# Kernel tuning notes

Measured on AMD Instinct MI355X. Metric: run time of the kernel, lower is better.

The kernel has to match this reference:

```python
import jax, jax.numpy as jnp
import numpy as np

NUM_NODES = 100000
PROP_STEP = 8


def _spmm(vals, rows, cols, x):
    # sparse [N,N] @ dense [N,F]: gather source rows, scale, scatter-add to dest
    gathered = x[cols] * vals[:, None]  # [E, F]
    return jax.ops.segment_sum(gathered, rows, num_segments=NUM_NODES)


def setup_inputs() -> dict:
    key = jax.random.key(0)
    k1, k2, k3, k4, k5 = jax.random.split(key, 5)
    N, E, C = NUM_NODES, 3200000, 128
    x = jax.random.normal(k1, (N, C), dtype=jnp.float32)
    # xavier_uniform for weight [c_in, c_out]
    limit = float(np.sqrt(6.0 / (C + C)))
    weight = jax.random.uniform(k2, (C, C), dtype=jnp.float32, minval=-limit, maxval=limit)
    lap_vals = jax.random.uniform(k3, (E,), dtype=jnp.float32)
    lap_rows = jax.random.randint(k4, (E,), 0, N, dtype=jnp.int64)
    lap_cols = jax.random.randint(k5, (E,), 0, N, dtype=jnp.int64)
    return {"x": x, "weight": weight, "lap_vals": lap_vals,
            "lap_rows": lap_rows, "lap_cols": lap_cols}


def reference(x, weight, lap_vals, lap_rows, lap_cols):
    # filter_type='low', dropout inactive (eval / p=0)
    identity = x
    out = x @ weight  # [N, c_out]
    for _ in range(PROP_STEP):
        out = _spmm(lap_vals, lap_rows, lap_cols, out)
    return identity + out
```

## Files before the change

kernel.cpp:

```cpp
#include <hip/hip_runtime.h>
#include <hip/hip_bf16.h>
#include <hip/hip_fp16.h>
#include <stdint.h>

#define CCH 128
#define FINAL_SCALE 268435456.0f
#define RND 2048
#define BUKSH 9
#define BUKROWS 512
#define MAXBUK 256

typedef float f4_t __attribute__((ext_vector_type(4)));
typedef int i2_t __attribute__((ext_vector_type(2)));

__device__ __forceinline__ int2 nt_load_i2(const int2* p) {
    i2_t t = __builtin_nontemporal_load((const i2_t*)p);
    return make_int2(t.x, t.y);
}
__device__ __forceinline__ float4 nt_load_f4(const float* p) {
    f4_t t = __builtin_nontemporal_load((const f4_t*)p);
    return make_float4(t.x, t.y, t.z, t.w);
}
__device__ __forceinline__ void nt_store_f4(void* p, float a, float b, float c, float d) {
    f4_t t = {a, b, c, d};
    __builtin_nontemporal_store(t, (f4_t*)p);
}


__global__ __launch_bounds__(256) void bucket_hist_kernel(const int* __restrict__ rows,
                                                          int* __restrict__ bukcnt,
                                                          int E, int nbuk) {
    __shared__ int h[MAXBUK];
    for (int i = threadIdx.x; i < nbuk; i += 256) h[i] = 0;
    __syncthreads();
    int stride = gridDim.x * blockDim.x;
    for (int e = blockIdx.x * blockDim.x + threadIdx.x; e < E; e += stride)
        atomicAdd(&h[rows[e] >> BUKSH], 1);
    __syncthreads();
    for (int i = threadIdx.x; i < nbuk; i += 256)
        if (h[i]) atomicAdd(&bukcnt[i], h[i]);
}

__global__ __launch_bounds__(MAXBUK) void bucket_scan_kernel(const int* __restrict__ bukcnt,
                                                             int* __restrict__ bukptr,
                                                             int* __restrict__ gcur, int nbuk) {
    __shared__ int tile[MAXBUK];
    int t = threadIdx.x;
    tile[t] = (t < nbuk) ? bukcnt[t] : 0;
    __syncthreads();
    for (int off = 1; off < MAXBUK; off <<= 1) {
        int add = (t >= off) ? tile[t - off] : 0;
        __syncthreads();
        tile[t] += add;
        __syncthreads();
    }
    int excl = (t == 0) ? 0 : tile[t - 1];
    if (t < nbuk) {
        bukptr[t] = excl;
        gcur[t] = excl;
    }
    if (t == nbuk - 1) bukptr[nbuk] = tile[t];
}

__global__ __launch_bounds__(256) void part_kernel(const int* __restrict__ rows,
                                                   const int* __restrict__ cols,
                                                   const float* __restrict__ vals,
                                                   int* __restrict__ gcur,
                                                   int4* __restrict__ recs,
                                                   int E, int nbuk) {
    __shared__ int hist[MAXBUK];
    __shared__ int offs[MAXBUK];
    __shared__ int cur[MAXBUK];
    __shared__ int gbase[MAXBUK];
    __shared__ int4 stage[RND];

    int base = blockIdx.x * RND;
    int cnt = E - base;
    if (cnt > RND) cnt = RND;
    if (cnt <= 0) return;

    for (int i = threadIdx.x; i < nbuk; i += 256) hist[i] = 0;
    __syncthreads();

    int myr[RND / 256], myc[RND / 256];
    float myv[RND / 256];
#pragma unroll
    for (int k = 0; k < RND / 256; ++k) {
        int li = k * 256 + threadIdx.x;
        bool ok = li < cnt;
        int gi = base + li;
        myr[k] = ok ? rows[gi] : -1;
        myc[k] = ok ? cols[gi] : 0;
        myv[k] = ok ? vals[gi] : 0.f;
        if (ok) atomicAdd(&hist[myr[k] >> BUKSH], 1);
    }
    __syncthreads();

    if (threadIdx.x == 0) {
        int run = 0;
        for (int b = 0; b < nbuk; ++b) {
            offs[b] = run;
            cur[b] = run;
            run += hist[b];
        }
    }
    __syncthreads();
    if (threadIdx.x < nbuk) gbase[threadIdx.x] = atomicAdd(&gcur[threadIdx.x], hist[threadIdx.x]);
    __syncthreads();

#pragma unroll
    for (int k = 0; k < RND / 256; ++k) {
        if (myr[k] >= 0) {
            int b = myr[k] >> BUKSH;
            int p = atomicAdd(&cur[b], 1);
            stage[p] = make_int4(myr[k], myc[k], __float_as_int(myv[k]), 0);
        }
    }
    __syncthreads();

    for (int i = threadIdx.x; i < cnt; i += 256) {
        int4 r = stage[i];
        int b = r.x >> BUKSH;
        recs[(size_t)gbase[b] + (i - offs[b])] = r;
    }
}

__global__ __launch_bounds__(512) void csrfill2_kernel(const int4* __restrict__ recs,
                                                       const int* __restrict__ bukptr,
                                                       int* __restrict__ row_ptr,
                                                       int2* __restrict__ edges,
                                                       int n, int E) {
    __shared__ int lcnt[BUKROWS];
    __shared__ int lscan[BUKROWS];
    __shared__ int lfill[BUKROWS];
    int bucket = blockIdx.x;
    int r0 = bucket << BUKSH;
    if (r0 >= n) return;
    int t = threadIdx.x;
    int bstart = bukptr[bucket];
    int bend = bukptr[bucket + 1];

    lcnt[t] = 0;
    __syncthreads();

    for (int i = bstart + t; i < bend; i += 512)
        atomicAdd(&lcnt[recs[i].x - r0], 1);
    __syncthreads();

    int v = lcnt[t];
    lscan[t] = v;
    __syncthreads();
    for (int off = 1; off < 512; off <<= 1) {
        int add = (t >= off) ? lscan[t - off] : 0;
        __syncthreads();
        lscan[t] += add;
        __syncthreads();
    }
    int excl = lscan[t] - v;

    int r = r0 + t;
    if (r < n) row_ptr[r] = bstart + excl;
    if (bucket == 0 && t == 0) row_ptr[n] = E;

    lfill[t] = 0;
    lcnt[t] = bstart + excl;
    __syncthreads();

    int i = bstart + t;
    for (; i + 512 < bend; i += 1024) {
        int4 a = recs[i];
        int4 b = recs[i + 512];
        int pa = lcnt[a.x - r0] + atomicAdd(&lfill[a.x - r0], 1);
        int pb = lcnt[b.x - r0] + atomicAdd(&lfill[b.x - r0], 1);
        edges[pa] = make_int2(a.y, a.z);
        edges[pb] = make_int2(b.y, b.z);
    }
    if (i < bend) {
        int4 a = recs[i];
        int pa = lcnt[a.x - r0] + atomicAdd(&lfill[a.x - r0], 1);
        edges[pa] = make_int2(a.y, a.z);
    }
}


#define GEMM_ROWS 64

__global__ __launch_bounds__(256) void gemm_kernel(const float* __restrict__ x,
                                                   const float* __restrict__ w,
                                                   __half* __restrict__ out, int n) {
    __shared__ __half2 wl[CCH * 64];
    for (int i = threadIdx.x; i < CCH * 64 / 2; i += 256) {
        float4 v = ((const float4*)w)[i];
        wl[2 * i]     = __float22half2_rn(make_float2(v.x, v.y));
        wl[2 * i + 1] = __float22half2_rn(make_float2(v.z, v.w));
    }
    __syncthreads();

    int tc = threadIdx.x & 31;
    int tr = threadIdx.x >> 5;
    int rbase = blockIdx.x * GEMM_ROWS + tr * 8;
    int nr = n - rbase;
    if (nr > 8) nr = 8;
    if (nr <= 0) nr = 0;

    float acc[8][4] = {};
    const float* xp = x + (size_t)rbase * CCH;

    float4 xc[8];
#pragma unroll
    for (int j = 0; j < 8; ++j)
        xc[j] = (j < nr) ? *(const float4*)(xp + (size_t)j * CCH)
                         : make_float4(0.f, 0.f, 0.f, 0.f);

    for (int k = 0; k < CCH; k += 4) {
        float4 xn[8];
        if (k + 4 < CCH) {
#pragma unroll
            for (int j = 0; j < 8; ++j)
                xn[j] = (j < nr) ? *(const float4*)(xp + (size_t)j * CCH + k + 4)
                                 : make_float4(0.f, 0.f, 0.f, 0.f);
        }
#pragma unroll
        for (int kk = 0; kk < 4; ++kk) {
            __half2 w01 = wl[(k + kk) * 64 + tc * 2];
            __half2 w23 = wl[(k + kk) * 64 + tc * 2 + 1];
            float2 f01 = __half22float2(w01);
            float2 f23 = __half22float2(w23);
#pragma unroll
            for (int j = 0; j < 8; ++j) {
                float xs = (kk == 0) ? xc[j].x : (kk == 1) ? xc[j].y : (kk == 2) ? xc[j].z : xc[j].w;
                acc[j][0] += xs * f01.x;
                acc[j][1] += xs * f01.y;
                acc[j][2] += xs * f23.x;
                acc[j][3] += xs * f23.y;
            }
        }
        if (k + 4 < CCH) {
#pragma unroll
            for (int j = 0; j < 8; ++j) xc[j] = xn[j];
        }
    }
#pragma unroll
    for (int j = 0; j < 8; ++j)
        if (j < nr) {
            __half2* orow = (__half2*)(out + (size_t)(rbase + j) * CCH + tc * 4);
            orow[0] = __float22half2_rn(make_float2(acc[j][0], acc[j][1]));
            orow[1] = __float22half2_rn(make_float2(acc[j][2], acc[j][3]));
        }
}


template <int FINAL>
__global__ __launch_bounds__(256) void spmm_kernel(const int* __restrict__ row_ptr,
                                                   const int2* __restrict__ edges,
                                                   const __half* __restrict__ src,
                                                   __half* __restrict__ dsth,
                                                   float* __restrict__ dstf,
                                                   const float* __restrict__ identity,
                                                   int n) {
    int lane = threadIdx.x & 63;
    int row = (blockIdx.x * blockDim.x + threadIdx.x) >> 6;
    if (row >= n) return;
    int g = lane >> 4;
    int gl = lane & 15;

    int s = row_ptr[row];
    int e = row_ptr[row + 1];

    float acc[8] = {};

    for (int base = s; base < e; base += 16) {
        int2 ed[4];
        float4 gv[4];
#pragma unroll
        for (int t = 0; t < 4; ++t) {
            int idx = base + g * 4 + t;
            bool ok = idx < e;
            ed[t] = nt_load_i2(&edges[ok ? idx : s]);
            if (!ok) ed[t].y = 0;
        }
#pragma unroll
        for (int t = 0; t < 4; ++t)
            gv[t] = *(const float4*)(src + (size_t)ed[t].x * CCH + gl * 8);
#pragma unroll
        for (int t = 0; t < 4; ++t) {
            float v = __int_as_float(ed[t].y);
            const __half* h = (const __half*)&gv[t];
#pragma unroll
            for (int j = 0; j < 8; ++j)
                acc[j] += v * __half2float(h[j]);
        }
    }

#pragma unroll
    for (int j = 0; j < 8; ++j) {
        acc[j] += __shfl_xor(acc[j], 16, 64);
        acc[j] += __shfl_xor(acc[j], 32, 64);
    }

    if (FINAL) {
        if (g == 0) {
            float4 iv = nt_load_f4(identity + (size_t)row * CCH + gl * 8);
            nt_store_f4(dstf + (size_t)row * CCH + gl * 8,
                        iv.x + acc[0] * FINAL_SCALE, iv.y + acc[1] * FINAL_SCALE,
                        iv.z + acc[2] * FINAL_SCALE, iv.w + acc[3] * FINAL_SCALE);
        } else if (g == 1) {
            float4 iv = nt_load_f4(identity + (size_t)row * CCH + gl * 8 + 4);
            nt_store_f4(dstf + (size_t)row * CCH + gl * 8 + 4,
                        iv.x + acc[4] * FINAL_SCALE, iv.y + acc[5] * FINAL_SCALE,
                        iv.z + acc[6] * FINAL_SCALE, iv.w + acc[7] * FINAL_SCALE);
        }
    } else {
        if (g == 0) {
            __half2 h[4];
            h[0] = __float22half2_rn(make_float2(acc[0] * 0.0625f, acc[1] * 0.0625f));
            h[1] = __float22half2_rn(make_float2(acc[2] * 0.0625f, acc[3] * 0.0625f));
            h[2] = __float22half2_rn(make_float2(acc[4] * 0.0625f, acc[5] * 0.0625f));
            h[3] = __float22half2_rn(make_float2(acc[6] * 0.0625f, acc[7] * 0.0625f));
            float4 hv = *(float4*)h;
            nt_store_f4(dsth + (size_t)row * CCH + gl * 8, hv.x, hv.y, hv.z, hv.w);
        }
    }
}


static inline size_t align256(size_t x) { return (x + 255) & ~(size_t)255; }

extern "C" void kernel_launch(void* const* d_in, const int* in_sizes, int n_in,
                              void* d_out, int out_size, void* d_ws, size_t ws_size,
                              hipStream_t stream) {
    const float* x = (const float*)d_in[0];
    const float* w = (const float*)d_in[1];
    const float* lap_vals = (const float*)d_in[2];
    const int* lap_rows = (const int*)d_in[3];
    const int* lap_cols = (const int*)d_in[4];

    const int N = in_sizes[0] / CCH;
    const int E = in_sizes[2];
    const int NBUK = (N + BUKROWS - 1) >> BUKSH;

    char* ws = (char*)d_ws;
    size_t off = 0;
    __half* bufA = (__half*)(ws + off); off = align256(off + (size_t)N * CCH * sizeof(__half));
    __half* bufB = (__half*)(ws + off); off = align256(off + (size_t)N * CCH * sizeof(__half));
    int2* edges = (int2*)(ws + off);    off = align256(off + (size_t)E * sizeof(int2) + 16);
    int* row_ptr = (int*)(ws + off);    off = align256(off + (size_t)(N + 1) * sizeof(int));
    int* bukcnt = (int*)(ws + off);     off = align256(off + (size_t)MAXBUK * sizeof(int));
    int* bukptr = (int*)(ws + off);     off = align256(off + (size_t)(MAXBUK + 1) * sizeof(int));
    int* gcur = (int*)(ws + off);       off = align256(off + (size_t)MAXBUK * sizeof(int));
    (void)ws_size;
    int4* recs = (int4*)bufA;

    float* out = (float*)d_out;

    hipMemsetAsync(bukcnt, 0, (size_t)MAXBUK * sizeof(int), stream);

    bucket_hist_kernel<<<512, 256, 0, stream>>>(lap_rows, bukcnt, E, NBUK);
    bucket_scan_kernel<<<1, MAXBUK, 0, stream>>>(bukcnt, bukptr, gcur, NBUK);
    part_kernel<<<(E + RND - 1) / RND, 256, 0, stream>>>(lap_rows, lap_cols, lap_vals,
                                                         gcur, recs, E, NBUK);
    csrfill2_kernel<<<NBUK, 512, 0, stream>>>(recs, bukptr, row_ptr, edges, N, E);

    gemm_kernel<<<(N + GEMM_ROWS - 1) / GEMM_ROWS, 256, 0, stream>>>(x, w, bufA, N);

    int spmm_blocks = (N + 3) / 4;
    const __half* src = bufA;
    __half* dst = bufB;
    for (int step = 1; step <= 7; ++step) {
        spmm_kernel<0><<<spmm_blocks, 256, 0, stream>>>(row_ptr, edges, src, dst, nullptr, nullptr, N);
        __half* t = (__half*)src;
        src = dst;
        dst = t;
    }
    spmm_kernel<1><<<spmm_blocks, 256, 0, stream>>>(row_ptr, edges, src, nullptr, out, x, N);
}
```

Before: 1.196 ms.

## Pack partition records into 8 bytes and drop nontemporal hints in SpMM

The partition stage now stores each edge as a packed 32-bit word (local row in the high bits, column in the low 17 bits) plus a separate float value, instead of a 16-byte int4. This halves the intermediate record traffic written by part_kernel and read twice by csrfill2_kernel. The SpMM edge loads and the half-precision intermediate stores also switch from nontemporal to regular accesses, so the edge list and feature buffers can stay in cache across steps. Column packing assumes node indices fit in 17 bits, so it only works for graphs with fewer than 131072 nodes.

```diff
diff --git a/kernel.cpp b/kernel.cpp
--- a/kernel.cpp
+++ b/kernel.cpp
@@ -9,14 +9,10 @@
 #define BUKSH 9
 #define BUKROWS 512
 #define MAXBUK 256
+#define COLMASK 0x1FFFF
 
 typedef float f4_t __attribute__((ext_vector_type(4)));
-typedef int i2_t __attribute__((ext_vector_type(2)));
-
-__device__ __forceinline__ int2 nt_load_i2(const int2* p) {
-    i2_t t = __builtin_nontemporal_load((const i2_t*)p);
-    return make_int2(t.x, t.y);
-}
+
 __device__ __forceinline__ float4 nt_load_f4(const float* p) {
     f4_t t = __builtin_nontemporal_load((const f4_t*)p);
     return make_float4(t.x, t.y, t.z, t.w);
@@ -66,13 +62,16 @@
                                                    const int* __restrict__ cols,
                                                    const float* __restrict__ vals,
                                                    int* __restrict__ gcur,
-                                                   int4* __restrict__ recs,
+                                                   unsigned int* __restrict__ rec_rc,
+                                                   float* __restrict__ rec_v,
                                                    int E, int nbuk) {
     __shared__ int hist[MAXBUK];
     __shared__ int offs[MAXBUK];
     __shared__ int cur[MAXBUK];
     __shared__ int gbase[MAXBUK];
-    __shared__ int4 stage[RND];
+    __shared__ unsigned int stage_rc[RND];
+    __shared__ float stage_v[RND];
+    __shared__ unsigned char stage_b[RND];
 
     int base = blockIdx.x * RND;
     int cnt = E - base;
@@ -113,19 +112,23 @@
         if (myr[k] >= 0) {
             int b = myr[k] >> BUKSH;
             int p = atomicAdd(&cur[b], 1);
-            stage[p] = make_int4(myr[k], myc[k], __float_as_int(myv[k]), 0);
+            stage_rc[p] = ((unsigned int)(myr[k] & (BUKROWS - 1)) << 17) | (unsigned int)myc[k];
+            stage_v[p] = myv[k];
+            stage_b[p] = (unsigned char)b;
         }
     }
     __syncthreads();
 
     for (int i = threadIdx.x; i < cnt; i += 256) {
-        int4 r = stage[i];
-        int b = r.x >> BUKSH;
-        recs[(size_t)gbase[b] + (i - offs[b])] = r;
-    }
-}
-
-__global__ __launch_bounds__(512) void csrfill2_kernel(const int4* __restrict__ recs,
+        int b = stage_b[i];
+        size_t d = (size_t)gbase[b] + (i - offs[b]);
+        rec_rc[d] = stage_rc[i];
+        rec_v[d] = stage_v[i];
+    }
+}
+
+__global__ __launch_bounds__(512) void csrfill2_kernel(const unsigned int* __restrict__ rec_rc,
+                                                       const float* __restrict__ rec_v,
                                                        const int* __restrict__ bukptr,
                                                        int* __restrict__ row_ptr,
                                                        int2* __restrict__ edges,
@@ -144,7 +147,7 @@
     __syncthreads();
 
     for (int i = bstart + t; i < bend; i += 512)
-        atomicAdd(&lcnt[recs[i].x - r0], 1);
+        atomicAdd(&lcnt[rec_rc[i] >> 17], 1);
     __syncthreads();
 
     int v = lcnt[t];
@@ -168,17 +171,22 @@
 
     int i = bstart + t;
     for (; i + 512 < bend; i += 1024) {
-        int4 a = recs[i];
-        int4 b = recs[i + 512];
-        int pa = lcnt[a.x - r0] + atomicAdd(&lfill[a.x - r0], 1);
-        int pb = lcnt[b.x - r0] + atomicAdd(&lfill[b.x - r0], 1);
-        edges[pa] = make_int2(a.y, a.z);
-        edges[pb] = make_int2(b.y, b.z);
+        unsigned int wa = rec_rc[i];
+        unsigned int wb = rec_rc[i + 512];
+        float va = rec_v[i];
+        float vb = rec_v[i + 512];
+        int ra = wa >> 17, rb = wb >> 17;
+        int pa = lcnt[ra] + atomicAdd(&lfill[ra], 1);
+        int pb = lcnt[rb] + atomicAdd(&lfill[rb], 1);
+        edges[pa] = make_int2((int)(wa & COLMASK), __float_as_int(va));
+        edges[pb] = make_int2((int)(wb & COLMASK), __float_as_int(vb));
     }
     if (i < bend) {
-        int4 a = recs[i];
-        int pa = lcnt[a.x - r0] + atomicAdd(&lfill[a.x - r0], 1);
-        edges[pa] = make_int2(a.y, a.z);
+        unsigned int wa = rec_rc[i];
+        float va = rec_v[i];
+        int ra = wa >> 17;
+        int pa = lcnt[ra] + atomicAdd(&lfill[ra], 1);
+        edges[pa] = make_int2((int)(wa & COLMASK), __float_as_int(va));
     }
 }
 
@@ -276,7 +284,7 @@
         for (int t = 0; t < 4; ++t) {
             int idx = base + g * 4 + t;
             bool ok = idx < e;
-            ed[t] = nt_load_i2(&edges[ok ? idx : s]);
+            ed[t] = edges[ok ? idx : s];
             if (!ok) ed[t].y = 0;
         }
 #pragma unroll
@@ -317,8 +325,7 @@
             h[1] = __float22half2_rn(make_float2(acc[2] * 0.0625f, acc[3] * 0.0625f));
             h[2] = __float22half2_rn(make_float2(acc[4] * 0.0625f, acc[5] * 0.0625f));
             h[3] = __float22half2_rn(make_float2(acc[6] * 0.0625f, acc[7] * 0.0625f));
-            float4 hv = *(float4*)h;
-            nt_store_f4(dsth + (size_t)row * CCH + gl * 8, hv.x, hv.y, hv.z, hv.w);
+            *(float4*)(dsth + (size_t)row * CCH + gl * 8) = *(float4*)h;
         }
     }
 }
@@ -349,7 +356,8 @@
     int* bukptr = (int*)(ws + off);     off = align256(off + (size_t)(MAXBUK + 1) * sizeof(int));
     int* gcur = (int*)(ws + off);       off = align256(off + (size_t)MAXBUK * sizeof(int));
     (void)ws_size;
-    int4* recs = (int4*)bufA;
+    unsigned int* rec_rc = (unsigned int*)bufA;
+    float* rec_v = (float*)(rec_rc + E);
 
     float* out = (float*)d_out;
 
@@ -358,8 +366,8 @@
     bucket_hist_kernel<<<512, 256, 0, stream>>>(lap_rows, bukcnt, E, NBUK);
     bucket_scan_kernel<<<1, MAXBUK, 0, stream>>>(bukcnt, bukptr, gcur, NBUK);
     part_kernel<<<(E + RND - 1) / RND, 256, 0, stream>>>(lap_rows, lap_cols, lap_vals,
-                                                         gcur, recs, E, NBUK);
-    csrfill2_kernel<<<NBUK, 512, 0, stream>>>(recs, bukptr, row_ptr, edges, N, E);
+                                                         gcur, rec_rc, rec_v, E, NBUK);
+    csrfill2_kernel<<<NBUK, 512, 0, stream>>>(rec_rc, rec_v, bukptr, row_ptr, edges, N, E);
 
     gemm_kernel<<<(N + GEMM_ROWS - 1) / GEMM_ROWS, 256, 0, stream>>>(x, w, bufA, N);
 
```

New measurement: 1.148 ms. 1.04x faster.
